# Performance work log

Measured on AMD Instinct MI355X. Metric: run time of the kernel, lower is better.

The kernel has to match this reference:

```python
import jax, jax.numpy as jnp
import numpy as np

B, SEQ_LEN, N_VARS, N_MARK = 16, 96, 862, 4
D_MODEL, D_STATE, D_CONV, D_FF = 512, 16, 2, 512
DT_RANK = 32  # ceil(d_model/16)
E_LAYERS = 2
PRED_LEN = 96
EPS = 1e-5


def _layer_norm(x, w, b):
    mu = x.mean(-1, keepdims=True)
    var = ((x - mu) ** 2).mean(-1, keepdims=True)
    return (x - mu) / jnp.sqrt(var + EPS) * w + b


def _selective_scan(xc, dt, Bm, Cm, A, D):
    # xc, dt: [B,S,d]; Bm, Cm: [B,S,ds]; A: [d,ds]; D: [d]
    def step(h, inp):
        x_t, dt_t, B_t, C_t = inp  # [B,d],[B,d],[B,ds],[B,ds]
        dA = jnp.exp(dt_t[..., None] * A)                      # [B,d,ds]
        h = dA * h + (dt_t * x_t)[..., None] * B_t[:, None, :]
        return h, jnp.einsum('bds,bs->bd', h, C_t)
    h0 = jnp.zeros((xc.shape[0], A.shape[0], A.shape[1]), xc.dtype)
    xs = tuple(jnp.swapaxes(t, 0, 1) for t in (xc, dt, Bm, Cm))
    _, ys = jax.lax.scan(step, h0, xs)
    return jnp.swapaxes(ys, 0, 1) + xc * D


def _mamba(x, in_W, conv_W, conv_b, xproj_W, dt_W, dt_b, A_log, D, out_W):
    d = in_W.shape[0] // 2
    xz = x @ in_W.T                                             # [B,S,2d]
    xi, z = xz[..., :d], xz[..., d:]
    xp = jnp.pad(xi, ((0, 0), (1, 0), (0, 0)))                  # causal pad, d_conv=2
    xc = xp[:, :-1] * conv_W[:, 0] + xp[:, 1:] * conv_W[:, 1] + conv_b
    xc = jax.nn.silu(xc)
    dbc = xc @ xproj_W.T                                        # [B,S,dt_rank+2*ds]
    dtr = dbc[..., :DT_RANK]
    Bm = dbc[..., DT_RANK:DT_RANK + D_STATE]
    Cm = dbc[..., DT_RANK + D_STATE:]
    dt = jax.nn.softplus(dtr @ dt_W.T + dt_b)
    A = -jnp.exp(A_log)
    y = _selective_scan(xc, dt, Bm, Cm, A, D)
    return (y * jax.nn.silu(z)) @ out_W.T


def _forward(x_enc, x_mark_enc, emb_W, emb_b,
             mf_in_W, mf_conv_W, mf_conv_b, mf_xproj_W, mf_dt_W, mf_dt_b, mf_A_log, mf_D, mf_out_W,
             mr_in_W, mr_conv_W, mr_conv_b, mr_xproj_W, mr_dt_W, mr_dt_b, mr_A_log, mr_D, mr_out_W,
             conv1_W, conv1_b, conv2_W, conv2_b, ln1_w, ln1_b, ln2_w, ln2_b,
             enc_norm_w, enc_norm_b, proj_W, proj_b):
    # RevIN-style instance normalization over time
    means = x_enc.mean(1, keepdims=True)
    xe = x_enc - means
    stdev = jnp.sqrt(jnp.mean(xe ** 2, axis=1, keepdims=True) + EPS)  # unbiased=False
    xe = xe / stdev
    N = x_enc.shape[2]
    # inverted embedding: variates (+ time marks) are tokens, Linear over time axis
    tok = jnp.concatenate([jnp.swapaxes(xe, 1, 2), jnp.swapaxes(x_mark_enc, 1, 2)], axis=1)
    x = tok @ emb_W.T + emb_b                                   # [B, N+4, d_model]
    for l in range(E_LAYERS):
        fwd = _mamba(x, mf_in_W[l], mf_conv_W[l], mf_conv_b[l], mf_xproj_W[l],
                     mf_dt_W[l], mf_dt_b[l], mf_A_log[l], mf_D[l], mf_out_W[l])
        rev = _mamba(x[:, ::-1], mr_in_W[l], mr_conv_W[l], mr_conv_b[l], mr_xproj_W[l],
                     mr_dt_W[l], mr_dt_b[l], mr_A_log[l], mr_D[l], mr_out_W[l])[:, ::-1]
        x = x + fwd + rev
        y = x = _layer_norm(x, ln1_w[l], ln1_b[l])
        y = jax.nn.relu(y @ conv1_W[l].T + conv1_b[l])          # 1x1 conv == linear
        y = y @ conv2_W[l].T + conv2_b[l]
        x = _layer_norm(x + y, ln2_w[l], ln2_b[l])
    x = _layer_norm(x, enc_norm_w, enc_norm_b)
    dec = jnp.swapaxes(x @ proj_W.T + proj_b, 1, 2)[:, :, :N]   # [B, pred_len, N]
    dec = dec * stdev[:, 0][:, None, :] + means[:, 0][:, None, :]
    return dec


def setup_inputs() -> dict:
    key = jax.random.key(0)
    ks = iter(jax.random.split(key, 64))
    nrm = lambda shape, s=0.02: jax.random.normal(next(ks), shape, jnp.float32) * s
    inp = {
        'x_enc': jax.random.normal(next(ks), (B, SEQ_LEN, N_VARS), jnp.float32),
        'x_mark_enc': jax.random.normal(next(ks), (B, SEQ_LEN, N_MARK), jnp.float32),
        'x_dec': jnp.zeros((1, 1, 1), jnp.float32),
        'x_mark_dec': jnp.zeros((1, 1, 1), jnp.float32),
        'emb_W': nrm((D_MODEL, SEQ_LEN)),
        'emb_b': jnp.zeros((D_MODEL,), jnp.float32),
    }
    for p in ('mf', 'mr'):
        inp[p + '_in_W'] = nrm((E_LAYERS, 2 * D_MODEL, D_MODEL))
        inp[p + '_conv_W'] = nrm((E_LAYERS, D_MODEL, D_CONV), 0.1)
        inp[p + '_conv_b'] = jnp.zeros((E_LAYERS, D_MODEL), jnp.float32)
        inp[p + '_xproj_W'] = nrm((E_LAYERS, DT_RANK + 2 * D_STATE, D_MODEL))
        inp[p + '_dt_W'] = nrm((E_LAYERS, D_MODEL, DT_RANK), 0.1)
        inp[p + '_dt_b'] = nrm((E_LAYERS, D_MODEL), 0.1)
        inp[p + '_A_log'] = jnp.log(jnp.broadcast_to(
            jnp.arange(1, D_STATE + 1, dtype=jnp.float32), (E_LAYERS, D_MODEL, D_STATE)))
        inp[p + '_D'] = jnp.ones((E_LAYERS, D_MODEL), jnp.float32)
        inp[p + '_out_W'] = nrm((E_LAYERS, D_MODEL, D_MODEL))
    inp['conv1_W'] = nrm((E_LAYERS, D_FF, D_MODEL))
    inp['conv1_b'] = jnp.zeros((E_LAYERS, D_FF), jnp.float32)
    inp['conv2_W'] = nrm((E_LAYERS, D_MODEL, D_FF))
    inp['conv2_b'] = jnp.zeros((E_LAYERS, D_MODEL), jnp.float32)
    inp['ln1_w'] = jnp.ones((E_LAYERS, D_MODEL), jnp.float32)
    inp['ln1_b'] = jnp.zeros((E_LAYERS, D_MODEL), jnp.float32)
    inp['ln2_w'] = jnp.ones((E_LAYERS, D_MODEL), jnp.float32)
    inp['ln2_b'] = jnp.zeros((E_LAYERS, D_MODEL), jnp.float32)
    inp['enc_norm_w'] = jnp.ones((D_MODEL,), jnp.float32)
    inp['enc_norm_b'] = jnp.zeros((D_MODEL,), jnp.float32)
    inp['proj_W'] = nrm((PRED_LEN, D_MODEL))
    inp['proj_b'] = jnp.zeros((PRED_LEN,), jnp.float32)
    return inp


def reference(x_enc, x_mark_enc, x_dec, x_mark_dec, emb_W, emb_b,
              mf_in_W, mf_conv_W, mf_conv_b, mf_xproj_W, mf_dt_W, mf_dt_b, mf_A_log, mf_D, mf_out_W,
              mr_in_W, mr_conv_W, mr_conv_b, mr_xproj_W, mr_dt_W, mr_dt_b, mr_A_log, mr_D, mr_out_W,
              conv1_W, conv1_b, conv2_W, conv2_b, ln1_w, ln1_b, ln2_w, ln2_b,
              enc_norm_w, enc_norm_b, proj_W, proj_b):
    return _forward(x_enc, x_mark_enc, emb_W, emb_b,
                    mf_in_W, mf_conv_W, mf_conv_b, mf_xproj_W, mf_dt_W, mf_dt_b, mf_A_log, mf_D, mf_out_W,
                    mr_in_W, mr_conv_W, mr_conv_b, mr_xproj_W, mr_dt_W, mr_dt_b, mr_A_log, mr_D, mr_out_W,
                    conv1_W, conv1_b, conv2_W, conv2_b, ln1_w, ln1_b, ln2_w, ln2_b,
                    enc_norm_w, enc_norm_b, proj_W, proj_b)
```

## Files before the change

### kernel.cpp

```cpp
#include <hip/hip_runtime.h>
#include <math.h>

#define BATCH   16
#define SEQ     96
#define NVARS   862
#define NMARK   4
#define LTOK    866
#define MROWS   (BATCH*LTOK)
#define DM      512
#define DSTATE  16
#define DTRANK  32
#define DFF     512
#define PRED    96
#define EPS_F   1e-5f

#define CCH     32
#define TCH     28

typedef __attribute__((ext_vector_type(4))) float f32x4;
typedef __attribute__((ext_vector_type(8))) short bf16x8;
typedef unsigned short ushort_t;

__device__ __forceinline__ short f2bf(float f) {
    unsigned u = __builtin_bit_cast(unsigned, f);
    u += 0x7fffu + ((u >> 16) & 1u);
    return (short)(u >> 16);
}
__device__ __forceinline__ float bf2f(ushort_t u) {
    return __builtin_bit_cast(float, (unsigned)u << 16);
}

__global__ __launch_bounds__(256) void gemm_bf16(
    const ushort_t* __restrict__ A, int lda,
    const ushort_t* __restrict__ W, int ldw,
    const float* __restrict__ bias,
    const float* __restrict__ res,
    float* __restrict__ out, int ldo,
    int M, int N, int K, int act, int final_mode, int gx,
    const float* __restrict__ fstd, const float* __restrict__ fmean)
{
    __shared__ ushort_t Als[128 * 32];
    __shared__ ushort_t Bls[128 * 32];
    const int tid  = threadIdx.x;
    const int lane = tid & 63;
    const int w    = tid >> 6;
    const int wm   = w >> 1;
    const int wn   = w & 1;

    const int nwg = gridDim.x;
    const int orig = blockIdx.x;
    const int q = nwg >> 3, r = nwg & 7;
    const int xcd = orig & 7, idx = orig >> 3;
    const int swz = (xcd < r ? xcd * (q + 1) : r * (q + 1) + (xcd - r) * q) + idx;
    const int m0 = (swz / gx) * 128, n0 = (swz % gx) * 128;

    const int srow = tid >> 1;
    const int sh   = tid & 1;
    int gm = m0 + srow; if (gm > M - 1) gm = M - 1;
    const size_t aoff = (size_t)gm * lda + sh * 16;
    int gn = n0 + srow; if (gn > N - 1) gn = N - 1;
    const size_t woff = (size_t)gn * ldw + sh * 16;
    const int swz0 = ((sh * 2 + 0) ^ ((srow >> 1) & 3)) * 8;
    const int swz1 = ((sh * 2 + 1) ^ ((srow >> 1) & 3)) * 8;
    ushort_t* Awp = &Als[srow * 32];
    ushort_t* Bwp = &Bls[srow * 32];

    f32x4 acc[4][4];
#pragma unroll
    for (int i = 0; i < 4; ++i)
#pragma unroll
        for (int j = 0; j < 4; ++j) { f32x4 z = {0.f, 0.f, 0.f, 0.f}; acc[i][j] = z; }

    const int fr = lane & 15;
    const int kg = lane >> 4;
    const int cg = (kg ^ ((fr >> 1) & 3)) * 8;

    bf16x8 a0 = *(const bf16x8*)(A + aoff);
    bf16x8 a1 = *(const bf16x8*)(A + aoff + 8);
    bf16x8 b0 = *(const bf16x8*)(W + woff);
    bf16x8 b1 = *(const bf16x8*)(W + woff + 8);

    for (int k0 = 0; k0 < K; k0 += 32) {
        __syncthreads();
        *(bf16x8*)(Awp + swz0) = a0;
        *(bf16x8*)(Awp + swz1) = a1;
        *(bf16x8*)(Bwp + swz0) = b0;
        *(bf16x8*)(Bwp + swz1) = b1;
        __syncthreads();

        const int kn = (k0 + 32 < K) ? (k0 + 32) : k0;
        a0 = *(const bf16x8*)(A + aoff + kn);
        a1 = *(const bf16x8*)(A + aoff + kn + 8);
        b0 = *(const bf16x8*)(W + woff + kn);
        b1 = *(const bf16x8*)(W + woff + kn + 8);

        bf16x8 a4[4], b4[4];
#pragma unroll
        for (int i = 0; i < 4; ++i) {
            a4[i] = *(const bf16x8*)&Als[(wm * 64 + i * 16 + fr) * 32 + cg];
            b4[i] = *(const bf16x8*)&Bls[(wn * 64 + i * 16 + fr) * 32 + cg];
        }
#pragma unroll
        for (int mi = 0; mi < 4; ++mi)
#pragma unroll
            for (int ni = 0; ni < 4; ++ni)
                acc[mi][ni] = __builtin_amdgcn_mfma_f32_16x16x32_bf16(
                    a4[mi], b4[ni], acc[mi][ni], 0, 0, 0);
    }

#pragma unroll
    for (int mi = 0; mi < 4; ++mi) {
#pragma unroll
        for (int ni = 0; ni < 4; ++ni) {
            const int gnn = n0 + wn * 64 + ni * 16 + fr;
            if (gnn >= N) continue;
#pragma unroll
            for (int j = 0; j < 4; ++j) {
                const int gmm = m0 + wm * 64 + mi * 16 + kg * 4 + j;
                if (gmm >= M) continue;
                float v = acc[mi][ni][j];
                if (bias) v += bias[gnn];
                if (act == 1) v = fmaxf(v, 0.f);
                else if (act == 2) v = (v > 20.f) ? v : log1pf(__expf(v));
                if (res) v += res[(size_t)gmm * DM + gnn];
                if (!final_mode) {
                    out[(size_t)gmm * ldo + gnn] = v;
                } else {
                    const int bb = gmm / LTOK, vv = gmm - bb * LTOK;
                    if (vv < NVARS) {
                        out[((size_t)bb * PRED + gnn) * NVARS + vv] =
                            v * fstd[bb * NVARS + vv] + fmean[bb * NVARS + vv];
                    }
                }
            }
        }
    }
}

__global__ void cast_kernel(const float* __restrict__ src, ushort_t* __restrict__ dst, int n)
{
    for (int i = blockIdx.x * blockDim.x + threadIdx.x; i < n; i += gridDim.x * blockDim.x)
        dst[i] = (ushort_t)f2bf(src[i]);
}

__global__ void cvtcat_kernel(const float* __restrict__ fa, const float* __restrict__ fb,
                              ushort_t* __restrict__ dst, int n_elems)
{
    int i = blockIdx.x * blockDim.x + threadIdx.x;
    if (i >= n_elems) return;
    int n = i >> 10, k = i & 1023;
    float v = (k < 512) ? fa[n * 512 + k] : fb[n * 512 + (k - 512)];
    dst[i] = (ushort_t)f2bf(v);
}

struct CvtJobs {
    const float* src[12];
    ushort_t*    dst[12];
    int          n[12];
};
__global__ void cvt_kernel(CvtJobs jobs) {
    const int j = blockIdx.y;
    const float* s = jobs.src[j];
    ushort_t* d = jobs.dst[j];
    const int n = jobs.n[j];
    for (int i = blockIdx.x * blockDim.x + threadIdx.x; i < n; i += gridDim.x * blockDim.x)
        d[i] = (ushort_t)f2bf(s[i]);
}

__global__ void stats_kernel(const float* __restrict__ x_enc,
                             float* __restrict__ means, float* __restrict__ stdev)
{
    int i = blockIdx.x * blockDim.x + threadIdx.x;
    if (i >= BATCH * NVARS) return;
    int b = i / NVARS, v = i - b * NVARS;
    const float* p = x_enc + (size_t)b * SEQ * NVARS + v;
    float s = 0.f;
    for (int t = 0; t < SEQ; ++t) s += p[(size_t)t * NVARS];
    float mu = s / (float)SEQ;
    float ss = 0.f;
    for (int t = 0; t < SEQ; ++t) { float d = p[(size_t)t * NVARS] - mu; ss += d * d; }
    means[i] = mu;
    stdev[i] = sqrtf(ss / (float)SEQ + EPS_F);
}

__global__ void tok_kernel(const float* __restrict__ x_enc, const float* __restrict__ x_mark,
                           const float* __restrict__ means, const float* __restrict__ stdev,
                           ushort_t* __restrict__ tok)
{
    int i = blockIdx.x * blockDim.x + threadIdx.x;
    if (i >= MROWS * SEQ) return;
    int s = i % SEQ;
    int row = i / SEQ;
    int b = row / LTOK, l = row - b * LTOK;
    float val;
    if (l < NVARS) {
        val = (x_enc[((size_t)b * SEQ + s) * NVARS + l] - means[b * NVARS + l])
              / stdev[b * NVARS + l];
    } else {
        val = x_mark[((size_t)b * SEQ + s) * NMARK + (l - NVARS)];
    }
    tok[i] = (ushort_t)f2bf(val);
}

__global__ void conv_silu_kernel(const float* __restrict__ xz, float* __restrict__ xc,
                                 ushort_t* __restrict__ xc_bf,
                                 const float* __restrict__ cW, const float* __restrict__ cb,
                                 int dir)
{
    int i = blockIdx.x * blockDim.x + threadIdx.x;
    if (i >= MROWS * DM) return;
    int d = i & (DM - 1);
    int row = i >> 9;
    int t = row % LTOK;
    float cur = xz[(size_t)row * 1024 + d];
    float oth;
    if (dir == 0) oth = (t == 0)        ? 0.f : xz[(size_t)(row - 1) * 1024 + d];
    else          oth = (t == LTOK - 1) ? 0.f : xz[(size_t)(row + 1) * 1024 + d];
    float v = oth * cW[d * 2 + 0] + cur * cW[d * 2 + 1] + cb[d];
    float sv = v * (1.f / (1.f + __expf(-v)));
    xc[i] = sv;
    xc_bf[i] = (ushort_t)f2bf(sv);
}

__global__ __launch_bounds__(256) void scan1_kernel(
    const float* __restrict__ xc, const float* __restrict__ dt,
    const float* __restrict__ dbc, const float* __restrict__ A_log,
    float* __restrict__ aprod, float* __restrict__ hpart, int dir)
{
    __shared__ float Ls[TCH * 32];
    const int tid = threadIdx.x;
    const int d = blockIdx.x * 256 + tid;
    const int c = blockIdx.y;
    const int b = blockIdx.z;
    const int t0 = c * TCH;
    const int tend = min(t0 + TCH, LTOK);
    const size_t rowb = (size_t)b * LTOK;

    for (int i = tid; i < TCH * 32; i += 256) {
        const int tr = min(t0 + (i >> 5), LTOK - 1);
        Ls[i] = dbc[(rowb + tr) * 64 + 32 + (i & 31)];
    }
    __syncthreads();

    float Ads[16];
#pragma unroll
    for (int s = 0; s < 16; ++s) Ads[s] = -__expf(A_log[d * DSTATE + s]);
    float h[16];
#pragma unroll
    for (int s = 0; s < 16; ++s) h[s] = 0.f;
    float sumdt = 0.f;

    int t = dir ? tend - 1 : t0;
    const int step = dir ? -1 : 1;
    for (int it = 0; it < tend - t0; ++it, t += step) {
        const size_t row = rowb + t;
        const float dtv = dt[row * DM + d];
        const float xcv = xc[row * DM + d];
        const float du = dtv * xcv;
        sumdt += dtv;
        const float* Bp = &Ls[(t - t0) * 32];
#pragma unroll
        for (int s = 0; s < 16; ++s) {
            const float dA = __expf(dtv * Ads[s]);
            h[s] = dA * h[s] + du * Bp[s];
        }
    }
#pragma unroll
    for (int s = 0; s < 16; ++s) {
        const size_t oidx = ((size_t)(b * CCH + c) * 16 + s) * DM + d;
        aprod[oidx] = __expf(Ads[s] * sumdt);
        hpart[oidx] = h[s];
    }
}

__global__ __launch_bounds__(256) void scan2_kernel(
    float* __restrict__ aprod, const float* __restrict__ hpart, int dir)
{
    const int gid = blockIdx.x * 256 + threadIdx.x;
    const int d = gid & (DM - 1);
    const int s = (gid >> 9) & 15;
    const int b = gid >> 13;
    float h = 0.f;
    for (int ci = 0; ci < CCH; ++ci) {
        const int c = dir ? (CCH - 1 - ci) : ci;
        const size_t idxc = ((size_t)(b * CCH + c) * 16 + s) * DM + d;
        const float ap = aprod[idxc];
        const float hp = hpart[idxc];
        aprod[idxc] = h;
        h = hp + ap * h;
    }
}

__global__ __launch_bounds__(256) void scan3_kernel(
    const float* __restrict__ xc, const float* __restrict__ dt,
    const float* __restrict__ dbc, const float* __restrict__ xz,
    const float* __restrict__ A_log, const float* __restrict__ Dp,
    const float* __restrict__ hinit, ushort_t* __restrict__ ymcat, int dir)
{
    __shared__ float Ls[TCH * 32];
    const int tid = threadIdx.x;
    const int d = blockIdx.x * 256 + tid;
    const int c = blockIdx.y;
    const int b = blockIdx.z;
    const int t0 = c * TCH;
    const int tend = min(t0 + TCH, LTOK);
    const size_t rowb = (size_t)b * LTOK;

    for (int i = tid; i < TCH * 32; i += 256) {
        const int tr = min(t0 + (i >> 5), LTOK - 1);
        Ls[i] = dbc[(rowb + tr) * 64 + 32 + (i & 31)];
    }
    __syncthreads();

    float Ads[16];
#pragma unroll
    for (int s = 0; s < 16; ++s) Ads[s] = -__expf(A_log[d * DSTATE + s]);
    float h[16];
#pragma unroll
    for (int s = 0; s < 16; ++s)
        h[s] = hinit[((size_t)(b * CCH + c) * 16 + s) * DM + d];
    const float Dd = Dp[d];

    int t = dir ? tend - 1 : t0;
    const int step = dir ? -1 : 1;
    for (int it = 0; it < tend - t0; ++it, t += step) {
        const size_t row = rowb + t;
        const float dtv = dt[row * DM + d];
        const float xcv = xc[row * DM + d];
        const float du = dtv * xcv;
        const float* Bp = &Ls[(t - t0) * 32];
        float p0 = 0.f, p1 = 0.f, p2 = 0.f, p3 = 0.f;
#pragma unroll
        for (int s = 0; s < 16; ++s) {
            const float dA = __expf(dtv * Ads[s]);
            const float hn = dA * h[s] + du * Bp[s];
            h[s] = hn;
            const float pc = hn * Bp[16 + s];
            if ((s & 3) == 0) p0 += pc;
            else if ((s & 3) == 1) p1 += pc;
            else if ((s & 3) == 2) p2 += pc;
            else p3 += pc;
        }
        const float y = (p0 + p1) + (p2 + p3) + xcv * Dd;
        const float z = xz[row * 1024 + DM + d];
        ymcat[row * 1024 + dir * DM + d] =
            (ushort_t)f2bf(y * (z * (1.f / (1.f + __expf(-z)))));
    }
}

__global__ __launch_bounds__(256) void ln_kernel(const float* __restrict__ in,
                                                 const float* __restrict__ w,
                                                 const float* __restrict__ bp,
                                                 float* __restrict__ outf,
                                                 ushort_t* __restrict__ outb)
{
    const int row = blockIdx.x;
    const int tid = threadIdx.x;
    const float2 v = *(const float2*)(in + (size_t)row * DM + tid * 2);
    float s  = v.x + v.y;
    float ss = v.x * v.x + v.y * v.y;
    for (int off = 32; off; off >>= 1) {
        s  += __shfl_down(s, off);
        ss += __shfl_down(ss, off);
    }
    __shared__ float sh[10];
    const int wid = tid >> 6, lane = tid & 63;
    if (lane == 0) { sh[wid] = s; sh[4 + wid] = ss; }
    __syncthreads();
    if (tid == 0) {
        float S = sh[0] + sh[1] + sh[2] + sh[3];
        float SS = sh[4] + sh[5] + sh[6] + sh[7];
        float mu = S / (float)DM;
        float var = SS / (float)DM - mu * mu;
        sh[8] = mu; sh[9] = rsqrtf(var + EPS_F);
    }
    __syncthreads();
    const float mu = sh[8], rstd = sh[9];
    const int c = tid * 2;
    float2 o;
    o.x = (v.x - mu) * rstd * w[c]     + bp[c];
    o.y = (v.y - mu) * rstd * w[c + 1] + bp[c + 1];
    if (outf) *(float2*)(outf + (size_t)row * DM + c) = o;
    if (outb) {
        unsigned pk = (unsigned)(ushort_t)f2bf(o.x) | ((unsigned)(ushort_t)f2bf(o.y) << 16);
        ((unsigned*)outb)[(size_t)row * (DM / 2) + tid] = pk;
    }
}

static inline void launch_gemm(hipStream_t st, const ushort_t* A, int lda,
                               const ushort_t* W, int ldw, const float* bias,
                               const float* res, float* out, int ldo,
                               int M, int N, int K, int act, int fin = 0,
                               const float* fstd = nullptr, const float* fmean = nullptr)
{
    const int gx = (N + 127) / 128, gy = (M + 127) / 128;
    hipLaunchKernelGGL(gemm_bf16, dim3(gx * gy), dim3(256), 0, st,
                       A, lda, W, ldw, bias, res, out, ldo,
                       M, N, K, act, fin, gx, fstd, fmean);
}

extern "C" void kernel_launch(void* const* d_in, const int* in_sizes, int n_in,
                              void* d_out, int out_size, void* d_ws, size_t ws_size,
                              hipStream_t stream)
{
    const float* x_enc   = (const float*)d_in[0];
    const float* x_mark  = (const float*)d_in[1];
    const float* emb_W   = (const float*)d_in[4];
    const float* emb_b   = (const float*)d_in[5];
    const float* m_in_W[2]    = { (const float*)d_in[6],  (const float*)d_in[15] };
    const float* m_conv_W[2]  = { (const float*)d_in[7],  (const float*)d_in[16] };
    const float* m_conv_b[2]  = { (const float*)d_in[8],  (const float*)d_in[17] };
    const float* m_xproj_W[2] = { (const float*)d_in[9],  (const float*)d_in[18] };
    const float* m_dt_W[2]    = { (const float*)d_in[10], (const float*)d_in[19] };
    const float* m_dt_b[2]    = { (const float*)d_in[11], (const float*)d_in[20] };
    const float* m_A_log[2]   = { (const float*)d_in[12], (const float*)d_in[21] };
    const float* m_D[2]       = { (const float*)d_in[13], (const float*)d_in[22] };
    const float* m_out_W[2]   = { (const float*)d_in[14], (const float*)d_in[23] };
    const float* conv1_W = (const float*)d_in[24];
    const float* conv1_b = (const float*)d_in[25];
    const float* conv2_W = (const float*)d_in[26];
    const float* conv2_b = (const float*)d_in[27];
    const float* ln1_w = (const float*)d_in[28];
    const float* ln1_b = (const float*)d_in[29];
    const float* ln2_w = (const float*)d_in[30];
    const float* ln2_b = (const float*)d_in[31];
    const float* enc_w = (const float*)d_in[32];
    const float* enc_b = (const float*)d_in[33];
    const float* proj_W = (const float*)d_in[34];
    const float* proj_b = (const float*)d_in[35];

    const size_t MD = (size_t)MROWS * DM;
    float* ws = (float*)d_ws;
    size_t o = 0;
    float* means = ws + o; o += 13824;
    float* stdev = ws + o; o += 13824;
    float* xbuf  = ws + o; o += MD;
    float* accb  = ws + o; o += MD;
    float* xzb   = ws + o; o += 2 * MD;
    float* xcb   = ws + o; o += MD;
    float* dtb   = ws + o; o += MD;
    float* dbcb  = ws + o; o += (size_t)MROWS * 64;
    float* x2f   = xzb;
    float* hbuf  = xzb + MD;

    ushort_t* wsb = (ushort_t*)(ws + o);
    size_t so = 0;
    ushort_t* xbuf_bf = wsb + so; so += MD;
    ushort_t* ymcat   = wsb + so; so += 2 * MD;
    ushort_t* xcb_bf  = wsb + so; so += MD;
    ushort_t* x2_bf   = wsb + so; so += MD;
    ushort_t* dbcb_bf = wsb + so; so += (size_t)MROWS * 64;
    ushort_t* embW_bf = wsb + so; so += 49152;
    ushort_t* inW_bf[2];  inW_bf[0] = wsb + so; so += 1048576; inW_bf[1] = wsb + so; so += 1048576;
    ushort_t* xpW_bf[2];  xpW_bf[0] = wsb + so; so += 65536;   xpW_bf[1] = wsb + so; so += 65536;
    ushort_t* dtW_bf[2];  dtW_bf[0] = wsb + so; so += 32768;   dtW_bf[1] = wsb + so; so += 32768;
    ushort_t* outWcat[2]; outWcat[0] = wsb + so; so += 524288; outWcat[1] = wsb + so; so += 524288;
    ushort_t* c1W_bf = wsb + so; so += 524288;
    ushort_t* c2W_bf = wsb + so; so += 524288;
    ushort_t* projW_bf = wsb + so; so += 49152;
    ushort_t* tok_bf = x2_bf;
    ushort_t* hb_bf  = ymcat;
    float* aprod = (float*)xcb_bf;
    float* hpart = accb;

    CvtJobs jobs;
    jobs.src[0] = emb_W;        jobs.dst[0] = embW_bf;   jobs.n[0] = 49152;
    jobs.src[1] = m_in_W[0];    jobs.dst[1] = inW_bf[0]; jobs.n[1] = 1048576;
    jobs.src[2] = m_in_W[1];    jobs.dst[2] = inW_bf[1]; jobs.n[2] = 1048576;
    jobs.src[3] = m_xproj_W[0]; jobs.dst[3] = xpW_bf[0]; jobs.n[3] = 65536;
    jobs.src[4] = m_xproj_W[1]; jobs.dst[4] = xpW_bf[1]; jobs.n[4] = 65536;
    jobs.src[5] = m_dt_W[0];    jobs.dst[5] = dtW_bf[0]; jobs.n[5] = 32768;
    jobs.src[6] = m_dt_W[1];    jobs.dst[6] = dtW_bf[1]; jobs.n[6] = 32768;
    jobs.src[7] = conv1_W;      jobs.dst[7] = c1W_bf;    jobs.n[7] = 524288;
    jobs.src[8] = conv2_W;      jobs.dst[8] = c2W_bf;    jobs.n[8] = 524288;
    jobs.src[9] = proj_W;       jobs.dst[9] = projW_bf;  jobs.n[9] = 49152;
    jobs.src[10] = emb_W;       jobs.dst[10] = embW_bf;  jobs.n[10] = 0;
    jobs.src[11] = emb_W;       jobs.dst[11] = embW_bf;  jobs.n[11] = 0;
    hipLaunchKernelGGL(cvt_kernel, dim3(64, 12), dim3(256), 0, stream, jobs);
    for (int l = 0; l < 2; ++l)
        hipLaunchKernelGGL(cvtcat_kernel, dim3((512 * 1024 + 255) / 256), dim3(256), 0, stream,
                           m_out_W[0] + (size_t)l * DM * DM,
                           m_out_W[1] + (size_t)l * DM * DM,
                           outWcat[l], 512 * 1024);

    hipLaunchKernelGGL(stats_kernel, dim3((BATCH * NVARS + 255) / 256), dim3(256), 0, stream,
                       x_enc, means, stdev);
    hipLaunchKernelGGL(tok_kernel, dim3((MROWS * SEQ + 255) / 256), dim3(256), 0, stream,
                       x_enc, x_mark, means, stdev, tok_bf);
    launch_gemm(stream, tok_bf, SEQ, embW_bf, SEQ, emb_b, nullptr,
                xbuf, DM, MROWS, DM, SEQ, 0);
    hipLaunchKernelGGL(cast_kernel, dim3(2048), dim3(256), 0, stream,
                       xbuf, xbuf_bf, (int)MD);

    for (int l = 0; l < 2; ++l) {
        for (int dir = 0; dir < 2; ++dir) {
            const ushort_t* inW  = inW_bf[dir]  + (size_t)l * 2 * DM * DM;
            const float* cW   = m_conv_W[dir]  + (size_t)l * DM * 2;
            const float* cb   = m_conv_b[dir]  + (size_t)l * DM;
            const ushort_t* xpW  = xpW_bf[dir] + (size_t)l * 64 * DM;
            const ushort_t* dtW  = dtW_bf[dir] + (size_t)l * DM * DTRANK;
            const float* dtbias = m_dt_b[dir]  + (size_t)l * DM;
            const float* Alog = m_A_log[dir]   + (size_t)l * DM * DSTATE;
            const float* Dp   = m_D[dir]       + (size_t)l * DM;

            launch_gemm(stream, xbuf_bf, DM, inW, DM, nullptr, nullptr,
                        xzb, 1024, MROWS, 2 * DM, DM, 0);
            hipLaunchKernelGGL(conv_silu_kernel, dim3((MROWS * DM + 255) / 256), dim3(256),
                               0, stream, xzb, xcb, xcb_bf, cW, cb, dir);
            launch_gemm(stream, xcb_bf, DM, xpW, DM, nullptr, nullptr,
                        dbcb, 64, MROWS, 64, DM, 0);
            hipLaunchKernelGGL(cast_kernel, dim3(512), dim3(256), 0, stream,
                               dbcb, dbcb_bf, MROWS * 64);
            launch_gemm(stream, dbcb_bf, 64, dtW, DTRANK, dtbias, nullptr,
                        dtb, DM, MROWS, DM, DTRANK, 2);
            hipLaunchKernelGGL(scan1_kernel, dim3(2, CCH, BATCH), dim3(256), 0, stream,
                               xcb, dtb, dbcb, Alog, aprod, hpart, dir);
            hipLaunchKernelGGL(scan2_kernel, dim3((BATCH * 16 * DM) / 256), dim3(256), 0, stream,
                               aprod, hpart, dir);
            hipLaunchKernelGGL(scan3_kernel, dim3(2, CCH, BATCH), dim3(256), 0, stream,
                               xcb, dtb, dbcb, xzb, Alog, Dp, aprod, ymcat, dir);
        }
        launch_gemm(stream, ymcat, 1024, outWcat[l], 1024, nullptr,
                    xbuf, accb, DM, MROWS, DM, 1024, 0);
        hipLaunchKernelGGL(ln_kernel, dim3(MROWS), dim3(256), 0, stream,
                           accb, ln1_w + l * DM, ln1_b + l * DM, x2f, x2_bf);
        launch_gemm(stream, x2_bf, DM, c1W_bf + (size_t)l * DFF * DM, DM,
                    conv1_b + l * DFF, nullptr,
                    hbuf, DFF, MROWS, DFF, DM, 1);
        hipLaunchKernelGGL(cast_kernel, dim3(2048), dim3(256), 0, stream,
                           hbuf, hb_bf, (int)MD);
        launch_gemm(stream, hb_bf, DFF, c2W_bf + (size_t)l * DM * DFF, DFF,
                    conv2_b + l * DM, x2f,
                    accb, DM, MROWS, DM, DFF, 0);
        hipLaunchKernelGGL(ln_kernel, dim3(MROWS), dim3(256), 0, stream,
                           accb, ln2_w + l * DM, ln2_b + l * DM, xbuf, xbuf_bf);
    }

    hipLaunchKernelGGL(ln_kernel, dim3(MROWS), dim3(256), 0, stream,
                       xbuf, enc_w, enc_b, nullptr, x2_bf);
    launch_gemm(stream, x2_bf, DM, projW_bf, DM, proj_b, nullptr,
                (float*)d_out, 0, MROWS, PRED, DM, 0, 1, stdev, means);
}
```

Baseline: 1.718 ms.

## Fold dt projection into x_proj weights to fuse two GEMMs into one

Precomputes a composed weight dt_W·xproj_W[:32] and stacks it with the B/C rows of xproj_W into a 544x512 bf16 matrix. A single GEMM from xc then produces softplus(dt) and the B/C columns, replacing the xproj GEMM, a cast kernel and the dt GEMM on every mamba call. The cost is more FLOPs (N=544 instead of 64+512 at K=32), plus rounding differences because the low-rank intermediate is no longer rounded to bf16.

```diff
diff --git a/kernel.cpp b/kernel.cpp
--- a/kernel.cpp
+++ b/kernel.cpp
@@ -17,6 +17,8 @@
 #define CCH     32
 #define TCH     28
 
+#define NDTBC   (544 * 512)
+
 typedef __attribute__((ext_vector_type(4))) float f32x4;
 typedef __attribute__((ext_vector_type(8))) short bf16x8;
 typedef unsigned short ushort_t;
@@ -36,8 +38,9 @@
     const float* __restrict__ bias,
     const float* __restrict__ res,
     float* __restrict__ out, int ldo,
-    int M, int N, int K, int act, int final_mode, int gx,
-    const float* __restrict__ fstd, const float* __restrict__ fmean)
+    int M, int N, int K, int act, int mode, int gx,
+    const float* __restrict__ fstd, const float* __restrict__ fmean,
+    float* __restrict__ out2)
 {
     __shared__ ushort_t Als[128 * 32];
     __shared__ ushort_t Bls[128 * 32];
@@ -119,11 +122,21 @@
                 const int gmm = m0 + wm * 64 + mi * 16 + kg * 4 + j;
                 if (gmm >= M) continue;
                 float v = acc[mi][ni][j];
+                if (mode == 3) {
+                    if (gnn < DM) {
+                        float t = v + bias[gnn];
+                        t = (t > 20.f) ? t : log1pf(__expf(t));
+                        out[(size_t)gmm * DM + gnn] = t;
+                    } else {
+                        out2[(size_t)gmm * 32 + (gnn - DM)] = v;
+                    }
+                    continue;
+                }
                 if (bias) v += bias[gnn];
                 if (act == 1) v = fmaxf(v, 0.f);
                 else if (act == 2) v = (v > 20.f) ? v : log1pf(__expf(v));
                 if (res) v += res[(size_t)gmm * DM + gnn];
-                if (!final_mode) {
+                if (mode == 0) {
                     out[(size_t)gmm * ldo + gnn] = v;
                 } else {
                     const int bb = gmm / LTOK, vv = gmm - bb * LTOK;
@@ -153,10 +166,30 @@
     dst[i] = (ushort_t)f2bf(v);
 }
 
+__global__ void compose_dtbc_kernel(const float* __restrict__ dtW,
+                                    const float* __restrict__ xpW,
+                                    ushort_t* __restrict__ Wout)
+{
+    const int i = blockIdx.x * 256 + threadIdx.x;
+    if (i >= NDTBC) return;
+    const int n = i >> 9, k = i & 511;
+    float v;
+    if (n < 512) {
+        float acc = 0.f;
+#pragma unroll
+        for (int r = 0; r < 32; ++r)
+            acc = fmaf(dtW[n * 32 + r], xpW[r * 512 + k], acc);
+        v = acc;
+    } else {
+        v = xpW[(n - 512 + 32) * 512 + k];
+    }
+    Wout[i] = (ushort_t)f2bf(v);
+}
+
 struct CvtJobs {
-    const float* src[12];
-    ushort_t*    dst[12];
-    int          n[12];
+    const float* src[6];
+    ushort_t*    dst[6];
+    int          n[6];
 };
 __global__ void cvt_kernel(CvtJobs jobs) {
     const int j = blockIdx.y;
@@ -224,7 +257,7 @@
 
 __global__ __launch_bounds__(256) void scan1_kernel(
     const float* __restrict__ xc, const float* __restrict__ dt,
-    const float* __restrict__ dbc, const float* __restrict__ A_log,
+    const float* __restrict__ bc, const float* __restrict__ A_log,
     float* __restrict__ aprod, float* __restrict__ hpart, int dir)
 {
     __shared__ float Ls[TCH * 32];
@@ -238,7 +271,7 @@
 
     for (int i = tid; i < TCH * 32; i += 256) {
         const int tr = min(t0 + (i >> 5), LTOK - 1);
-        Ls[i] = dbc[(rowb + tr) * 64 + 32 + (i & 31)];
+        Ls[i] = bc[(rowb + tr) * 32 + (i & 31)];
     }
     __syncthreads();
 
@@ -293,7 +326,7 @@
 
 __global__ __launch_bounds__(256) void scan3_kernel(
     const float* __restrict__ xc, const float* __restrict__ dt,
-    const float* __restrict__ dbc, const float* __restrict__ xz,
+    const float* __restrict__ bc, const float* __restrict__ xz,
     const float* __restrict__ A_log, const float* __restrict__ Dp,
     const float* __restrict__ hinit, ushort_t* __restrict__ ymcat, int dir)
 {
@@ -308,7 +341,7 @@
 
     for (int i = tid; i < TCH * 32; i += 256) {
         const int tr = min(t0 + (i >> 5), LTOK - 1);
-        Ls[i] = dbc[(rowb + tr) * 64 + 32 + (i & 31)];
+        Ls[i] = bc[(rowb + tr) * 32 + (i & 31)];
     }
     __syncthreads();
 
@@ -390,13 +423,14 @@
 static inline void launch_gemm(hipStream_t st, const ushort_t* A, int lda,
                                const ushort_t* W, int ldw, const float* bias,
                                const float* res, float* out, int ldo,
-                               int M, int N, int K, int act, int fin = 0,
-                               const float* fstd = nullptr, const float* fmean = nullptr)
+                               int M, int N, int K, int act, int mode = 0,
+                               const float* fstd = nullptr, const float* fmean = nullptr,
+                               float* out2 = nullptr)
 {
     const int gx = (N + 127) / 128, gy = (M + 127) / 128;
     hipLaunchKernelGGL(gemm_bf16, dim3(gx * gy), dim3(256), 0, st,
                        A, lda, W, ldw, bias, res, out, ldo,
-                       M, N, K, act, fin, gx, fstd, fmean);
+                       M, N, K, act, mode, gx, fstd, fmean, out2);
 }
 
 extern "C" void kernel_launch(void* const* d_in, const int* in_sizes, int n_in,
@@ -439,7 +473,7 @@
     float* xzb   = ws + o; o += 2 * MD;
     float* xcb   = ws + o; o += MD;
     float* dtb   = ws + o; o += MD;
-    float* dbcb  = ws + o; o += (size_t)MROWS * 64;
+    float* bcb   = ws + o; o += (size_t)MROWS * 32;
     float* x2f   = xzb;
     float* hbuf  = xzb + MD;
 
@@ -449,11 +483,9 @@
     ushort_t* ymcat   = wsb + so; so += 2 * MD;
     ushort_t* xcb_bf  = wsb + so; so += MD;
     ushort_t* x2_bf   = wsb + so; so += MD;
-    ushort_t* dbcb_bf = wsb + so; so += (size_t)MROWS * 64;
     ushort_t* embW_bf = wsb + so; so += 49152;
     ushort_t* inW_bf[2];  inW_bf[0] = wsb + so; so += 1048576; inW_bf[1] = wsb + so; so += 1048576;
-    ushort_t* xpW_bf[2];  xpW_bf[0] = wsb + so; so += 65536;   xpW_bf[1] = wsb + so; so += 65536;
-    ushort_t* dtW_bf[2];  dtW_bf[0] = wsb + so; so += 32768;   dtW_bf[1] = wsb + so; so += 32768;
+    ushort_t* dtbcW   = wsb + so; so += 4 * NDTBC;
     ushort_t* outWcat[2]; outWcat[0] = wsb + so; so += 524288; outWcat[1] = wsb + so; so += 524288;
     ushort_t* c1W_bf = wsb + so; so += 524288;
     ushort_t* c2W_bf = wsb + so; so += 524288;
@@ -464,19 +496,20 @@
     float* hpart = accb;
 
     CvtJobs jobs;
-    jobs.src[0] = emb_W;        jobs.dst[0] = embW_bf;   jobs.n[0] = 49152;
-    jobs.src[1] = m_in_W[0];    jobs.dst[1] = inW_bf[0]; jobs.n[1] = 1048576;
-    jobs.src[2] = m_in_W[1];    jobs.dst[2] = inW_bf[1]; jobs.n[2] = 1048576;
-    jobs.src[3] = m_xproj_W[0]; jobs.dst[3] = xpW_bf[0]; jobs.n[3] = 65536;
-    jobs.src[4] = m_xproj_W[1]; jobs.dst[4] = xpW_bf[1]; jobs.n[4] = 65536;
-    jobs.src[5] = m_dt_W[0];    jobs.dst[5] = dtW_bf[0]; jobs.n[5] = 32768;
-    jobs.src[6] = m_dt_W[1];    jobs.dst[6] = dtW_bf[1]; jobs.n[6] = 32768;
-    jobs.src[7] = conv1_W;      jobs.dst[7] = c1W_bf;    jobs.n[7] = 524288;
-    jobs.src[8] = conv2_W;      jobs.dst[8] = c2W_bf;    jobs.n[8] = 524288;
-    jobs.src[9] = proj_W;       jobs.dst[9] = projW_bf;  jobs.n[9] = 49152;
-    jobs.src[10] = emb_W;       jobs.dst[10] = embW_bf;  jobs.n[10] = 0;
-    jobs.src[11] = emb_W;       jobs.dst[11] = embW_bf;  jobs.n[11] = 0;
-    hipLaunchKernelGGL(cvt_kernel, dim3(64, 12), dim3(256), 0, stream, jobs);
+    jobs.src[0] = emb_W;     jobs.dst[0] = embW_bf;   jobs.n[0] = 49152;
+    jobs.src[1] = m_in_W[0]; jobs.dst[1] = inW_bf[0]; jobs.n[1] = 1048576;
+    jobs.src[2] = m_in_W[1]; jobs.dst[2] = inW_bf[1]; jobs.n[2] = 1048576;
+    jobs.src[3] = conv1_W;   jobs.dst[3] = c1W_bf;    jobs.n[3] = 524288;
+    jobs.src[4] = conv2_W;   jobs.dst[4] = c2W_bf;    jobs.n[4] = 524288;
+    jobs.src[5] = proj_W;    jobs.dst[5] = projW_bf;  jobs.n[5] = 49152;
+    hipLaunchKernelGGL(cvt_kernel, dim3(64, 6), dim3(256), 0, stream, jobs);
+    for (int dir = 0; dir < 2; ++dir)
+        for (int l = 0; l < 2; ++l)
+            hipLaunchKernelGGL(compose_dtbc_kernel, dim3((NDTBC + 255) / 256), dim3(256),
+                               0, stream,
+                               m_dt_W[dir] + (size_t)l * DM * DTRANK,
+                               m_xproj_W[dir] + (size_t)l * 64 * DM,
+                               dtbcW + (size_t)(dir * 2 + l) * NDTBC);
     for (int l = 0; l < 2; ++l)
         hipLaunchKernelGGL(cvtcat_kernel, dim3((512 * 1024 + 255) / 256), dim3(256), 0, stream,
                            m_out_W[0] + (size_t)l * DM * DM,
@@ -497,28 +530,23 @@
             const ushort_t* inW  = inW_bf[dir]  + (size_t)l * 2 * DM * DM;
             const float* cW   = m_conv_W[dir]  + (size_t)l * DM * 2;
             const float* cb   = m_conv_b[dir]  + (size_t)l * DM;
-            const ushort_t* xpW  = xpW_bf[dir] + (size_t)l * 64 * DM;
-            const ushort_t* dtW  = dtW_bf[dir] + (size_t)l * DM * DTRANK;
             const float* dtbias = m_dt_b[dir]  + (size_t)l * DM;
             const float* Alog = m_A_log[dir]   + (size_t)l * DM * DSTATE;
             const float* Dp   = m_D[dir]       + (size_t)l * DM;
+            const ushort_t* Wdtbc = dtbcW + (size_t)(dir * 2 + l) * NDTBC;
 
             launch_gemm(stream, xbuf_bf, DM, inW, DM, nullptr, nullptr,
                         xzb, 1024, MROWS, 2 * DM, DM, 0);
             hipLaunchKernelGGL(conv_silu_kernel, dim3((MROWS * DM + 255) / 256), dim3(256),
                                0, stream, xzb, xcb, xcb_bf, cW, cb, dir);
-            launch_gemm(stream, xcb_bf, DM, xpW, DM, nullptr, nullptr,
-                        dbcb, 64, MROWS, 64, DM, 0);
-            hipLaunchKernelGGL(cast_kernel, dim3(512), dim3(256), 0, stream,
-                               dbcb, dbcb_bf, MROWS * 64);
-            launch_gemm(stream, dbcb_bf, 64, dtW, DTRANK, dtbias, nullptr,
-                        dtb, DM, MROWS, DM, DTRANK, 2);
+            launch_gemm(stream, xcb_bf, DM, Wdtbc, DM, dtbias, nullptr,
+                        dtb, DM, MROWS, 544, DM, 0, 3, nullptr, nullptr, bcb);
             hipLaunchKernelGGL(scan1_kernel, dim3(2, CCH, BATCH), dim3(256), 0, stream,
-                               xcb, dtb, dbcb, Alog, aprod, hpart, dir);
+                               xcb, dtb, bcb, Alog, aprod, hpart, dir);
             hipLaunchKernelGGL(scan2_kernel, dim3((BATCH * 16 * DM) / 256), dim3(256), 0, stream,
                                aprod, hpart, dir);
             hipLaunchKernelGGL(scan3_kernel, dim3(2, CCH, BATCH), dim3(256), 0, stream,
-                               xcb, dtb, dbcb, xzb, Alog, Dp, aprod, ymcat, dir);
+                               xcb, dtb, bcb, xzb, Alog, Dp, aprod, ymcat, dir);
         }
         launch_gemm(stream, ymcat, 1024, outWcat[l], 1024, nullptr,
                     xbuf, accb, DM, MROWS, DM, 1024, 0);
```

Result: faster. 1.630 ms (-5.1%).
